# Kernel tuning notes

Measured on AMD Instinct MI355X. Metric: run time of the kernel, lower is better.

The kernel has to match this reference:

```python
import jax, jax.numpy as jnp
import numpy as np

ASPECT_RATIOS = jnp.array([0.5, 1.0, 2.0], dtype=jnp.float32)
SCALES = jnp.array([1.0, 2.0, 4.0, 8.0, 16.0], dtype=jnp.float32)
BASE_SIZE = 16
STRIDE = 16
NEG_OVERLAP = 0.3
POS_OVERLAP = 0.7
PADDING = 0.0
RPN_BATCH = 256
RPN_FG_FRACTION = 0.5


def _mkanchors(ws, hs, x_ctr, y_ctr):
    return jnp.stack([x_ctr - 0.5 * (ws - 1), y_ctr - 0.5 * (hs - 1),
                      x_ctr + 0.5 * (ws - 1), y_ctr + 0.5 * (hs - 1)], axis=-1)


def _base_anchors():
    w = h = float(BASE_SIZE)
    x_ctr = y_ctr = 0.5 * (BASE_SIZE - 1)
    size = w * h
    size_ratios = size / ASPECT_RATIOS
    ws = jnp.round(jnp.sqrt(size_ratios))
    hs = jnp.round(ws * ASPECT_RATIOS)
    ratio_anchors = _mkanchors(ws, hs, x_ctr, y_ctr)          # (R,4)
    rw = ratio_anchors[:, 2] - ratio_anchors[:, 0] + 1
    rh = ratio_anchors[:, 3] - ratio_anchors[:, 1] + 1
    rx = ratio_anchors[:, 0] + 0.5 * (rw - 1)
    ry = ratio_anchors[:, 1] + 0.5 * (rh - 1)
    ws2 = rw[:, None] * SCALES[None, :]                        # (R,S)
    hs2 = rh[:, None] * SCALES[None, :]
    anchors = _mkanchors(ws2, hs2, rx[:, None], ry[:, None])   # (R,S,4)
    return anchors.reshape(-1, 4)                              # (A=R*S,4)


def _shifted_anchors(r, c):
    base = _base_anchors()                                     # (A,4)
    sx = jnp.arange(c, dtype=jnp.float32) * STRIDE
    sy = jnp.arange(r, dtype=jnp.float32) * STRIDE
    SX, SY = jnp.meshgrid(sx, sy)                              # (r,c)
    shifts = jnp.stack([SX.ravel(), SY.ravel(), SX.ravel(), SY.ravel()], axis=1)
    return (shifts[:, None, :] + base[None, :, :]).reshape(-1, 4)  # (K=r*c*A,4)


def _iou(a, b):
    area_a = (a[:, 2] - a[:, 0] + 1) * (a[:, 3] - a[:, 1] + 1)
    area_b = (b[:, 2] - b[:, 0] + 1) * (b[:, 3] - b[:, 1] + 1)
    iw = jnp.minimum(a[:, None, 2], b[None, :, 2]) - jnp.maximum(a[:, None, 0], b[None, :, 0]) + 1
    ih = jnp.minimum(a[:, None, 3], b[None, :, 3]) - jnp.maximum(a[:, None, 1], b[None, :, 1]) + 1
    inter = jnp.maximum(iw, 0) * jnp.maximum(ih, 0)
    return inter / (area_a[:, None] + area_b[None, :] - inter)


def _bbox_transform(ex, gt):
    ew = ex[:, 2] - ex[:, 0] + 1.0
    eh = ex[:, 3] - ex[:, 1] + 1.0
    ecx = ex[:, 0] + 0.5 * ew
    ecy = ex[:, 1] + 0.5 * eh
    gw = gt[:, 2] - gt[:, 0] + 1.0
    gh = gt[:, 3] - gt[:, 1] + 1.0
    gcx = gt[:, 0] + 0.5 * gw
    gcy = gt[:, 1] + 0.5 * gh
    return jnp.stack([(gcx - ecx) / ew, (gcy - ecy) / eh,
                      jnp.log(gw / ew), jnp.log(gh / eh)], axis=1)


def reference(target_bounding_boxes, metadata, scores):
    meta = metadata[0]
    gt = target_bounding_boxes[0]                               # (G,4)
    r, c = scores.shape[1], scores.shape[2]
    anchors = _shifted_anchors(r, c)                            # (K,4)
    K = anchors.shape[0]
    h, w = meta[0], meta[1]

    # anchors fully inside the image (padding=0); outside anchors masked
    inside = ((anchors[:, 0] >= -PADDING) & (anchors[:, 1] >= -PADDING) &
              (anchors[:, 2] < w + PADDING) & (anchors[:, 3] < h + PADDING))

    clipped = jnp.stack([jnp.clip(anchors[:, 0], 0.0, w - 1),
                         jnp.clip(anchors[:, 1], 0.0, h - 1),
                         jnp.clip(anchors[:, 2], 0.0, w - 1),
                         jnp.clip(anchors[:, 3], 0.0, h - 1)], axis=1)

    overlaps = _iou(clipped, gt)                                # (K,G)
    overlaps = jnp.where(inside[:, None], overlaps, -1.0)       # ignore outside anchors
    argmax_overlaps = jnp.argmax(overlaps, axis=1)              # best gt per anchor
    max_overlaps = jnp.max(overlaps, axis=1)
    gt_argmax = jnp.argmax(overlaps, axis=0)                    # best anchor per gt

    labels = jnp.full((K,), -1.0, dtype=jnp.float32)
    labels = jnp.where(inside & (max_overlaps < NEG_OVERLAP), 0.0, labels)
    labels = labels.at[gt_argmax].set(1.0)                      # dedup handled by .set
    labels = jnp.where(inside & (max_overlaps >= POS_OVERLAP), 1.0, labels)
    labels = jnp.where(inside, labels, -1.0)                    # unmap fill=-1

    # deterministic subsampling (original shuffles randomly): keep first-by-index
    num_fg = int(RPN_FG_FRACTION * RPN_BATCH)
    pos = labels == 1.0
    pos_rank = jnp.cumsum(pos.astype(jnp.int32))
    labels = jnp.where(pos & (pos_rank > num_fg), -1.0, labels)
    num_pos = jnp.minimum(pos.sum(), num_fg)
    num_bg = RPN_BATCH - num_pos
    neg = labels == 0.0
    neg_rank = jnp.cumsum(neg.astype(jnp.int32))
    labels = jnp.where(neg & (neg_rank > num_bg), -1.0, labels)

    matched_gt = gt[argmax_overlaps]                            # (K,4) gather
    bbox_targets = _bbox_transform(clipped, matched_gt)
    bbox_targets = jnp.where(inside[:, None], bbox_targets, 0.0)  # unmap fill=0

    return anchors[None], bbox_targets[None], labels[None]


def setup_inputs() -> dict:
    key = jax.random.key(0)
    k1, k2 = jax.random.split(key)
    H = W = 1600
    G = 100
    r = c = H // STRIDE                                          # 100
    A = 15                                                       # 3 ratios * 5 scales
    xy = jax.random.uniform(k1, (G, 2), minval=0.0, maxval=1400.0)
    wh = jax.random.uniform(k2, (G, 2), minval=16.0, maxval=200.0)
    gt = jnp.concatenate([xy, xy + wh], axis=1)[None]            # (1,G,4)
    metadata = jnp.array([[float(H), float(W), 1.0]], dtype=jnp.float32)
    scores = jnp.zeros((1, r, c, A), dtype=jnp.float32)          # only shape is used
    return {"target_bounding_boxes": gt, "metadata": metadata, "scores": scores}
```

## Files before the change

### kernel.cpp

```cpp
#include <hip/hip_runtime.h>
#include <math.h>


#define NUM_A 15
#define NUM_FG 128
#define RPN_BATCH 256
#define BLOCK 256
#define MAXG 256
#define SCAN_T 1024

__device__ __forceinline__ void base_anchor(int a, float& bx1, float& by1,
                                            float& bx2, float& by2) {
    const float RW[3] = {23.f, 16.f, 11.f};
    const float RH[3] = {12.f, 16.f, 22.f};
    int i = a / 5;
    int j = a - i * 5;
    float sc = (float)(1 << j);
    float w = RW[i] * sc;
    float h = RH[i] * sc;
    bx1 = 7.5f - 0.5f * (w - 1.f);
    by1 = 7.5f - 0.5f * (h - 1.f);
    bx2 = 7.5f + 0.5f * (w - 1.f);
    by2 = 7.5f + 0.5f * (h - 1.f);
}

__device__ __forceinline__ void anchor_coords(int k, int c, float& x1, float& y1,
                                              float& x2, float& y2) {
    int a = k % NUM_A;
    int p = k / NUM_A;
    int xi = p % c;
    int yi = p / c;
    float bx1, by1, bx2, by2;
    base_anchor(a, bx1, by1, bx2, by2);
    float sx = (float)xi * 16.f;
    float sy = (float)yi * 16.f;
    x1 = sx + bx1;  y1 = sy + by1;
    x2 = sx + bx2;  y2 = sy + by2;
}

__device__ __forceinline__ unsigned long long packvk(float v, int k) {
    unsigned u = __float_as_uint(v);
    u = (u & 0x80000000u) ? ~u : (u | 0x80000000u);
    return ((unsigned long long)u << 32) | (unsigned)(~k);
}

__global__ void __launch_bounds__(BLOCK) k_main(
        const float* __restrict__ gt, const float* __restrict__ meta,
        float* __restrict__ out_anch, float* __restrict__ out_bb,
        float* __restrict__ out_lab, int* __restrict__ posc, int* __restrict__ negc,
        unsigned long long* __restrict__ bestg, int K, int c, int G) {
    __shared__ float4 s_gt[MAXG];
    __shared__ unsigned long long s_best[MAXG];
    __shared__ int swp[4], swn[4];
    int tid = threadIdx.x;
    const float4* gtv = (const float4*)gt;
    for (int g = tid; g < G; g += BLOCK) {
        s_gt[g] = gtv[g];
        s_best[g] = 0ULL;
    }
    __syncthreads();

    int k = blockIdx.x * BLOCK + tid;
    bool valid = (k < K);
    float h = meta[0], w = meta[1];
    float wm1 = __fsub_rn(w, 1.f), hm1 = __fsub_rn(h, 1.f);

    float x1, y1, x2, y2;
    anchor_coords(k, c, x1, y1, x2, y2);
    if (valid) ((float4*)out_anch)[k] = make_float4(x1, y1, x2, y2);
    bool inside = (x1 >= 0.f) && (y1 >= 0.f) && (x2 < w) && (y2 < h);

    float cx1 = fminf(fmaxf(x1, 0.f), wm1);
    float cy1 = fminf(fmaxf(y1, 0.f), hm1);
    float cx2 = fminf(fmaxf(x2, 0.f), wm1);
    float cy2 = fminf(fmaxf(y2, 0.f), hm1);
    float area_a = __fmul_rn(__fadd_rn(__fsub_rn(cx2, cx1), 1.f),
                             __fadd_rn(__fsub_rn(cy2, cy1), 1.f));

    float maxv = -2.f;
    int arg = 0;
    if (valid && inside) {
        for (int g = 0; g < G; ++g) {
            float4 gb = gtv[g];
            float gw = __fadd_rn(__fsub_rn(gb.z, gb.x), 1.f);
            float gh = __fadd_rn(__fsub_rn(gb.w, gb.y), 1.f);
            float areab = __fmul_rn(gw, gh);
            float iw = __fadd_rn(__fsub_rn(fminf(cx2, gb.z), fmaxf(cx1, gb.x)), 1.f);
            float ih = __fadd_rn(__fsub_rn(fminf(cy2, gb.w), fmaxf(cy1, gb.y)), 1.f);
            float inter = __fmul_rn(fmaxf(iw, 0.f), fmaxf(ih, 0.f));
            float v = 0.f;
            if (inter > 0.f) {
                float denom = __fsub_rn(__fadd_rn(area_a, areab), inter);
                v = __fdiv_rn(inter, denom);
                atomicMax(&s_best[g], packvk(v, k));
            }
            if (v > maxv) { maxv = v; arg = g; }
        }
    }
    __syncthreads();
    for (int g = tid; g < G; g += BLOCK)
        if (s_best[g] != 0ULL) atomicMax(&bestg[g], s_best[g]);

    float labf = -1.f;
    if (valid) {
        float t0 = 0.f, t1 = 0.f, t2 = 0.f, t3 = 0.f;
        if (inside) {
            labf = (maxv >= 0.7f) ? 1.f : (maxv < 0.3f ? 0.f : -1.f);
            float4 gb = s_gt[arg];
            float ew  = __fadd_rn(__fsub_rn(cx2, cx1), 1.f);
            float eh  = __fadd_rn(__fsub_rn(cy2, cy1), 1.f);
            float ecx = __fadd_rn(cx1, __fmul_rn(0.5f, ew));
            float ecy = __fadd_rn(cy1, __fmul_rn(0.5f, eh));
            float gw  = __fadd_rn(__fsub_rn(gb.z, gb.x), 1.f);
            float gh  = __fadd_rn(__fsub_rn(gb.w, gb.y), 1.f);
            float gcx = __fadd_rn(gb.x, __fmul_rn(0.5f, gw));
            float gcy = __fadd_rn(gb.y, __fmul_rn(0.5f, gh));
            t0 = __fdiv_rn(__fsub_rn(gcx, ecx), ew);
            t1 = __fdiv_rn(__fsub_rn(gcy, ecy), eh);
            t2 = logf(__fdiv_rn(gw, ew));
            t3 = logf(__fdiv_rn(gh, eh));
        }
        ((float4*)out_bb)[k] = make_float4(t0, t1, t2, t3);
        out_lab[k] = labf;
    }

    bool pos = valid && (labf == 1.f);
    bool neg = valid && (labf == 0.f);
    unsigned long long bp = __ballot(pos ? 1 : 0);
    unsigned long long bn = __ballot(neg ? 1 : 0);
    int lane = tid & 63, wid = tid >> 6;
    if (lane == 0) { swp[wid] = __popcll(bp); swn[wid] = __popcll(bn); }
    __syncthreads();
    if (tid == 0) {
        posc[blockIdx.x] = swp[0] + swp[1] + swp[2] + swp[3];
        negc[blockIdx.x] = swn[0] + swn[1] + swn[2] + swn[3];
    }
}

__global__ void __launch_bounds__(SCAN_T) k_scan1(
        const unsigned long long* __restrict__ bestg, float* __restrict__ lab,
        int* __restrict__ posc, int* __restrict__ negc, int* __restrict__ numbg,
        int NB, int G) {
    __shared__ int sp[SCAN_T], sn[SCAN_T];
    __shared__ int s_k[MAXG];
    int tid = threadIdx.x;
    sp[tid] = (tid < NB) ? posc[tid] : 0;
    sn[tid] = (tid < NB) ? negc[tid] : 0;

    int kstar = -1;
    if (tid < G) {
        unsigned long long u = bestg[tid];
        if (u != 0ULL)
            kstar = (int)(~(unsigned)(u & 0xffffffffu));
    }
    if (tid < MAXG) s_k[tid] = kstar;
    __syncthreads();
    bool mine = (kstar >= 0);
    if (mine) {
        for (int j = 0; j < tid; ++j)
            if (s_k[j] == kstar) { mine = false; break; }
    }
    if (mine) {
        float oldl = lab[kstar];
        if (oldl != 1.f) {
            lab[kstar] = 1.f;
            int b = kstar / BLOCK;
            atomicAdd(&sp[b], 1);
            if (oldl == 0.f) atomicAdd(&sn[b], -1);
        }
    }
    __syncthreads();
    int op = sp[tid], on = sn[tid];
    int vp = op, vn = on;
    for (int off = 1; off < SCAN_T; off <<= 1) {
        int ap = 0, an = 0;
        if (tid >= off) { ap = sp[tid - off]; an = sn[tid - off]; }
        __syncthreads();
        vp += ap; vn += an;
        sp[tid] = vp; sn[tid] = vn;
        __syncthreads();
    }
    if (tid < NB) { posc[tid] = vp - op; negc[tid] = vn - on; }
    if (tid == 0) {
        int total_pos = sp[SCAN_T - 1];
        int np = total_pos < NUM_FG ? total_pos : NUM_FG;
        numbg[0] = RPN_BATCH - np;
    }
}

__global__ void __launch_bounds__(BLOCK) k_apply(
        float* __restrict__ lab, const int* __restrict__ posoff,
        const int* __restrict__ negoff, const int* __restrict__ numbg, int K) {
    __shared__ int swp[4], swn[4];
    int tid = threadIdx.x;
    int lane = tid & 63, wid = tid >> 6;
    unsigned long long lm = (1ULL << lane) - 1ULL;
    int k = blockIdx.x * BLOCK + tid;
    float lv = (k < K) ? lab[k] : -1.f;
    bool pos = (k < K) && (lv == 1.f);
    bool neg = (k < K) && (lv == 0.f);
    unsigned long long bp = __ballot(pos ? 1 : 0);
    unsigned long long bn = __ballot(neg ? 1 : 0);
    if (lane == 0) { swp[wid] = __popcll(bp); swn[wid] = __popcll(bn); }
    __syncthreads();
    int poff = 0, noff = 0;
    for (int wv = 0; wv < 4; ++wv)
        if (wv < wid) { poff += swp[wv]; noff += swn[wv]; }
    int prank = posoff[blockIdx.x] + poff + __popcll(bp & lm) + 1;
    int nrank = negoff[blockIdx.x] + noff + __popcll(bn & lm) + 1;
    int nb = numbg[0];
    if (pos && prank > NUM_FG) lab[k] = -1.f;
    if (neg && nrank > nb)     lab[k] = -1.f;
}

extern "C" void kernel_launch(void* const* d_in, const int* in_sizes, int n_in,
                              void* d_out, int out_size, void* d_ws, size_t ws_size,
                              hipStream_t stream) {
    const float* gt   = (const float*)d_in[0];
    const float* meta = (const float*)d_in[1];
    int G  = in_sizes[0] / 4;
    int rc = in_sizes[2] / NUM_A;
    int c = 1;
    while ((long long)(c + 1) * (c + 1) <= (long long)rc) ++c;
    int K  = rc * NUM_A;
    int NB = (K + BLOCK - 1) / BLOCK;

    float* out      = (float*)d_out;
    float* out_anch = out;
    float* out_bb   = out + (size_t)4 * K;
    float* out_lab  = out + (size_t)8 * K;

    unsigned long long* bestg = (unsigned long long*)d_ws;
    int* posc  = (int*)(bestg + MAXG);
    int* negc  = posc + SCAN_T;
    int* numbg = negc + SCAN_T;

    hipMemsetAsync(bestg, 0, MAXG * sizeof(unsigned long long), stream);
    hipLaunchKernelGGL(k_main, dim3(NB), dim3(BLOCK), 0, stream,
                       gt, meta, out_anch, out_bb, out_lab, posc, negc, bestg, K, c, G);
    hipLaunchKernelGGL(k_scan1, dim3(1), dim3(SCAN_T), 0, stream,
                       bestg, out_lab, posc, negc, numbg, NB, G);
    hipLaunchKernelGGL(k_apply, dim3(NB), dim3(BLOCK), 0, stream,
                       out_lab, posc, negc, numbg, K);
}
```

Before: 111.7 us.

## Fuse all stages into one cooperative kernel with grid syncs

Replaces the memset plus three kernel launches with a single cooperative kernel that uses grid-wide syncs between stages. Per-gt best anchors are written per block to a workspace and reduced by one block per gt, instead of global atomics. The IoU loop now reads gt boxes from shared memory, computes gt area only when boxes overlap, and skips the shared atomicMax when the current maximum is already higher. This trades launch overhead for grid barrier cost and needs all 586 blocks to be co-resident.

New measurement: 269.2 us. 141% more time.

```diff
diff --git a/kernel.cpp b/kernel.cpp
--- a/kernel.cpp
+++ b/kernel.cpp
@@ -1,5 +1,8 @@
 #include <hip/hip_runtime.h>
+#include <hip/hip_cooperative_groups.h>
 #include <math.h>
+
+namespace cg = cooperative_groups;
 
 
 #define NUM_A 15
@@ -7,7 +10,8 @@
 #define RPN_BATCH 256
 #define BLOCK 256
 #define MAXG 256
-#define SCAN_T 1024
+#define MAXNB 768
+#define CPT 3
 
 __device__ __forceinline__ void base_anchor(int a, float& bx1, float& by1,
                                             float& bx2, float& by2) {
@@ -44,23 +48,32 @@
     return ((unsigned long long)u << 32) | (unsigned)(~k);
 }
 
-__global__ void __launch_bounds__(BLOCK) k_main(
+__global__ void __launch_bounds__(BLOCK) k_all(
         const float* __restrict__ gt, const float* __restrict__ meta,
         float* __restrict__ out_anch, float* __restrict__ out_bb,
         float* __restrict__ out_lab, int* __restrict__ posc, int* __restrict__ negc,
-        unsigned long long* __restrict__ bestg, int K, int c, int G) {
+        unsigned long long* __restrict__ pbest, int* __restrict__ kstar,
+        int* __restrict__ numbg, int K, int c, int G, int NB) {
+    cg::grid_group grid = cg::this_grid();
     __shared__ float4 s_gt[MAXG];
     __shared__ unsigned long long s_best[MAXG];
+    __shared__ int s_adjp[MAXNB], s_adjn[MAXNB];
+    __shared__ int sp[BLOCK], sn[BLOCK];
+    __shared__ int s_k[MAXG];
     __shared__ int swp[4], swn[4];
+
     int tid = threadIdx.x;
+    int b = blockIdx.x;
+    int lane = tid & 63, wid = tid >> 6;
     const float4* gtv = (const float4*)gt;
+
     for (int g = tid; g < G; g += BLOCK) {
         s_gt[g] = gtv[g];
         s_best[g] = 0ULL;
     }
     __syncthreads();
 
-    int k = blockIdx.x * BLOCK + tid;
+    int k = b * BLOCK + tid;
     bool valid = (k < K);
     float h = meta[0], w = meta[1];
     float wm1 = __fsub_rn(w, 1.f), hm1 = __fsub_rn(h, 1.f);
@@ -81,25 +94,25 @@
     int arg = 0;
     if (valid && inside) {
         for (int g = 0; g < G; ++g) {
-            float4 gb = gtv[g];
-            float gw = __fadd_rn(__fsub_rn(gb.z, gb.x), 1.f);
-            float gh = __fadd_rn(__fsub_rn(gb.w, gb.y), 1.f);
-            float areab = __fmul_rn(gw, gh);
+            float4 gb = s_gt[g];
             float iw = __fadd_rn(__fsub_rn(fminf(cx2, gb.z), fmaxf(cx1, gb.x)), 1.f);
             float ih = __fadd_rn(__fsub_rn(fminf(cy2, gb.w), fmaxf(cy1, gb.y)), 1.f);
             float inter = __fmul_rn(fmaxf(iw, 0.f), fmaxf(ih, 0.f));
             float v = 0.f;
             if (inter > 0.f) {
+                float gw = __fadd_rn(__fsub_rn(gb.z, gb.x), 1.f);
+                float gh = __fadd_rn(__fsub_rn(gb.w, gb.y), 1.f);
+                float areab = __fmul_rn(gw, gh);
                 float denom = __fsub_rn(__fadd_rn(area_a, areab), inter);
                 v = __fdiv_rn(inter, denom);
-                atomicMax(&s_best[g], packvk(v, k));
+                unsigned long long pk = packvk(v, k);
+                unsigned cur_hi = ((volatile unsigned*)&s_best[g])[1];
+                if ((unsigned)(pk >> 32) >= cur_hi)
+                    atomicMax(&s_best[g], pk);
             }
             if (v > maxv) { maxv = v; arg = g; }
         }
     }
-    __syncthreads();
-    for (int g = tid; g < G; g += BLOCK)
-        if (s_best[g] != 0ULL) atomicMax(&bestg[g], s_best[g]);
 
     float labf = -1.f;
     if (valid) {
@@ -128,89 +141,119 @@
     bool neg = valid && (labf == 0.f);
     unsigned long long bp = __ballot(pos ? 1 : 0);
     unsigned long long bn = __ballot(neg ? 1 : 0);
-    int lane = tid & 63, wid = tid >> 6;
     if (lane == 0) { swp[wid] = __popcll(bp); swn[wid] = __popcll(bn); }
     __syncthreads();
     if (tid == 0) {
-        posc[blockIdx.x] = swp[0] + swp[1] + swp[2] + swp[3];
-        negc[blockIdx.x] = swn[0] + swn[1] + swn[2] + swn[3];
-    }
-}
-
-__global__ void __launch_bounds__(SCAN_T) k_scan1(
-        const unsigned long long* __restrict__ bestg, float* __restrict__ lab,
-        int* __restrict__ posc, int* __restrict__ negc, int* __restrict__ numbg,
-        int NB, int G) {
-    __shared__ int sp[SCAN_T], sn[SCAN_T];
-    __shared__ int s_k[MAXG];
-    int tid = threadIdx.x;
-    sp[tid] = (tid < NB) ? posc[tid] : 0;
-    sn[tid] = (tid < NB) ? negc[tid] : 0;
-
-    int kstar = -1;
-    if (tid < G) {
-        unsigned long long u = bestg[tid];
-        if (u != 0ULL)
-            kstar = (int)(~(unsigned)(u & 0xffffffffu));
-    }
-    if (tid < MAXG) s_k[tid] = kstar;
-    __syncthreads();
-    bool mine = (kstar >= 0);
-    if (mine) {
-        for (int j = 0; j < tid; ++j)
-            if (s_k[j] == kstar) { mine = false; break; }
-    }
-    if (mine) {
-        float oldl = lab[kstar];
-        if (oldl != 1.f) {
-            lab[kstar] = 1.f;
-            int b = kstar / BLOCK;
-            atomicAdd(&sp[b], 1);
-            if (oldl == 0.f) atomicAdd(&sn[b], -1);
-        }
-    }
-    __syncthreads();
-    int op = sp[tid], on = sn[tid];
-    int vp = op, vn = on;
-    for (int off = 1; off < SCAN_T; off <<= 1) {
-        int ap = 0, an = 0;
-        if (tid >= off) { ap = sp[tid - off]; an = sn[tid - off]; }
-        __syncthreads();
-        vp += ap; vn += an;
-        sp[tid] = vp; sn[tid] = vn;
-        __syncthreads();
-    }
-    if (tid < NB) { posc[tid] = vp - op; negc[tid] = vn - on; }
-    if (tid == 0) {
-        int total_pos = sp[SCAN_T - 1];
-        int np = total_pos < NUM_FG ? total_pos : NUM_FG;
-        numbg[0] = RPN_BATCH - np;
-    }
-}
-
-__global__ void __launch_bounds__(BLOCK) k_apply(
-        float* __restrict__ lab, const int* __restrict__ posoff,
-        const int* __restrict__ negoff, const int* __restrict__ numbg, int K) {
-    __shared__ int swp[4], swn[4];
-    int tid = threadIdx.x;
-    int lane = tid & 63, wid = tid >> 6;
-    unsigned long long lm = (1ULL << lane) - 1ULL;
-    int k = blockIdx.x * BLOCK + tid;
-    float lv = (k < K) ? lab[k] : -1.f;
-    bool pos = (k < K) && (lv == 1.f);
-    bool neg = (k < K) && (lv == 0.f);
-    unsigned long long bp = __ballot(pos ? 1 : 0);
-    unsigned long long bn = __ballot(neg ? 1 : 0);
-    if (lane == 0) { swp[wid] = __popcll(bp); swn[wid] = __popcll(bn); }
-    __syncthreads();
-    int poff = 0, noff = 0;
-    for (int wv = 0; wv < 4; ++wv)
-        if (wv < wid) { poff += swp[wv]; noff += swn[wv]; }
-    int prank = posoff[blockIdx.x] + poff + __popcll(bp & lm) + 1;
-    int nrank = negoff[blockIdx.x] + noff + __popcll(bn & lm) + 1;
-    int nb = numbg[0];
-    if (pos && prank > NUM_FG) lab[k] = -1.f;
-    if (neg && nrank > nb)     lab[k] = -1.f;
+        posc[b] = swp[0] + swp[1] + swp[2] + swp[3];
+        negc[b] = swn[0] + swn[1] + swn[2] + swn[3];
+    }
+    for (int g = tid; g < G; g += BLOCK)
+        pbest[(size_t)g * MAXNB + b] = s_best[g];
+
+    grid.sync();
+
+    if (b < G) {
+        unsigned long long v = 0ULL;
+        for (int i = tid; i < NB; i += BLOCK) {
+            unsigned long long u = pbest[(size_t)b * MAXNB + i];
+            if (u > v) v = u;
+        }
+        #pragma unroll
+        for (int off = 32; off > 0; off >>= 1) {
+            unsigned long long o = __shfl_down(v, off);
+            if (o > v) v = o;
+        }
+        if (lane == 0) s_best[wid] = v;
+        __syncthreads();
+        if (tid == 0) {
+            unsigned long long m = s_best[0];
+            for (int wv = 1; wv < 4; ++wv) if (s_best[wv] > m) m = s_best[wv];
+            kstar[b] = (m == 0ULL) ? -1 : (int)(~(unsigned)(m & 0xffffffffu));
+        }
+    }
+
+    grid.sync();
+
+    if (b == 0) {
+        for (int i = tid; i < MAXNB; i += BLOCK) { s_adjp[i] = 0; s_adjn[i] = 0; }
+        int lcp[CPT], lcn[CPT];
+        #pragma unroll
+        for (int j = 0; j < CPT; ++j) {
+            int e = tid * CPT + j;
+            lcp[j] = (e < NB) ? posc[e] : 0;
+            lcn[j] = (e < NB) ? negc[e] : 0;
+        }
+        s_k[tid] = (tid < G) ? kstar[tid] : -1;
+        __syncthreads();
+        int ks = s_k[tid];
+        bool mine = (ks >= 0);
+        if (mine) {
+            for (int j2 = 0; j2 < tid; ++j2)
+                if (s_k[j2] == ks) { mine = false; break; }
+        }
+        if (mine) {
+            float oldl = out_lab[ks];
+            if (oldl != 1.f) {
+                out_lab[ks] = 1.f;
+                int e = ks / BLOCK;
+                atomicAdd(&s_adjp[e], 1);
+                if (oldl == 0.f) atomicAdd(&s_adjn[e], -1);
+            }
+        }
+        __syncthreads();
+        int tp = 0, tn = 0;
+        #pragma unroll
+        for (int j = 0; j < CPT; ++j) {
+            int e = tid * CPT + j;
+            lcp[j] += s_adjp[e]; lcn[j] += s_adjn[e];
+            tp += lcp[j]; tn += lcn[j];
+        }
+        sp[tid] = tp; sn[tid] = tn;
+        __syncthreads();
+        int vp = tp, vn = tn;
+        for (int off = 1; off < BLOCK; off <<= 1) {
+            int ap = 0, an = 0;
+            if (tid >= off) { ap = sp[tid - off]; an = sn[tid - off]; }
+            __syncthreads();
+            vp += ap; vn += an;
+            sp[tid] = vp; sn[tid] = vn;
+            __syncthreads();
+        }
+        int runp = vp - tp, runn = vn - tn;
+        #pragma unroll
+        for (int j = 0; j < CPT; ++j) {
+            int e = tid * CPT + j;
+            if (e < NB) { posc[e] = runp; negc[e] = runn; }
+            runp += lcp[j]; runn += lcn[j];
+        }
+        if (tid == BLOCK - 1) {
+            int total_pos = vp;
+            int np = total_pos < NUM_FG ? total_pos : NUM_FG;
+            numbg[0] = RPN_BATCH - np;
+        }
+    }
+
+    grid.sync();
+
+    {
+        float lv = valid ? out_lab[k] : -1.f;
+        bool p4 = valid && (lv == 1.f);
+        bool n4 = valid && (lv == 0.f);
+        unsigned long long bp4 = __ballot(p4 ? 1 : 0);
+        unsigned long long bn4 = __ballot(n4 ? 1 : 0);
+        __syncthreads();
+        if (lane == 0) { swp[wid] = __popcll(bp4); swn[wid] = __popcll(bn4); }
+        __syncthreads();
+        int poff = 0, noff = 0;
+        for (int wv = 0; wv < 4; ++wv)
+            if (wv < wid) { poff += swp[wv]; noff += swn[wv]; }
+        unsigned long long lm = (1ULL << lane) - 1ULL;
+        int prank = posc[b] + poff + __popcll(bp4 & lm) + 1;
+        int nrank = negc[b] + noff + __popcll(bn4 & lm) + 1;
+        int nb = numbg[0];
+        if (p4 && prank > NUM_FG) out_lab[k] = -1.f;
+        if (n4 && nrank > nb)     out_lab[k] = -1.f;
+    }
 }
 
 extern "C" void kernel_launch(void* const* d_in, const int* in_sizes, int n_in,
@@ -230,16 +273,15 @@
     float* out_bb   = out + (size_t)4 * K;
     float* out_lab  = out + (size_t)8 * K;
 
-    unsigned long long* bestg = (unsigned long long*)d_ws;
-    int* posc  = (int*)(bestg + MAXG);
-    int* negc  = posc + SCAN_T;
-    int* numbg = negc + SCAN_T;
-
-    hipMemsetAsync(bestg, 0, MAXG * sizeof(unsigned long long), stream);
-    hipLaunchKernelGGL(k_main, dim3(NB), dim3(BLOCK), 0, stream,
-                       gt, meta, out_anch, out_bb, out_lab, posc, negc, bestg, K, c, G);
-    hipLaunchKernelGGL(k_scan1, dim3(1), dim3(SCAN_T), 0, stream,
-                       bestg, out_lab, posc, negc, numbg, NB, G);
-    hipLaunchKernelGGL(k_apply, dim3(NB), dim3(BLOCK), 0, stream,
-                       out_lab, posc, negc, numbg, K);
-}
+    unsigned long long* pbest = (unsigned long long*)d_ws;
+    int* kstar = (int*)(pbest + (size_t)MAXG * MAXNB);
+    int* posc  = kstar + MAXG;
+    int* negc  = posc + MAXNB;
+    int* numbg = negc + MAXNB;
+
+    void* args[] = {(void*)&gt, (void*)&meta, (void*)&out_anch, (void*)&out_bb,
+                    (void*)&out_lab, (void*)&posc, (void*)&negc, (void*)&pbest,
+                    (void*)&kstar, (void*)&numbg, (void*)&K, (void*)&c,
+                    (void*)&G, (void*)&NB};
+    hipLaunchCooperativeKernel((void*)k_all, dim3(NB), dim3(BLOCK), args, 0, stream);
+}
```
